# Performance work log

Measured on AMD Instinct MI355X. Metric: run time of the kernel, lower is better.

Reference implementation:

```python
import jax, jax.numpy as jnp
import numpy as np

BITS = 50

def _xor(a, b):
    # binary XOR on {0,1} floats: a + b - 2ab
    return a + b - 2.0 * a * b

def _maj(a, b, c):
    # majority (carry-out of a full adder) on {0,1} floats
    return a * b + a * c + b * c - 2.0 * a * b * c

def setup_inputs() -> dict:
    key = jax.random.key(0)
    kA, kB = jax.random.split(key)
    N = 1_000_000
    A = jax.random.randint(kA, (N, BITS), 0, 2).astype(jnp.float32)
    B = jax.random.randint(kB, (N, BITS), 0, 2).astype(jnp.float32)
    return {"A": A, "B": B}

def reference(A, B):
    """A - B via two's complement ripple-carry: A + NOT(B) + 1, LSB first.
    Returns (result [..., 50], borrow [..., 1])."""
    not_b = 1.0 - B                      # VecNOT
    # scan over the 50 bits (sequential carry dependency)
    a_bits = jnp.moveaxis(A, -1, 0)      # [50, N]
    b_bits = jnp.moveaxis(not_b, -1, 0)  # [50, N]
    c0 = jnp.ones(A.shape[:-1], dtype=A.dtype)  # initial carry = 1

    def step(c, ab):
        a, b = ab
        s = _xor(_xor(a, b), c)          # FullAdder sum
        c_next = _maj(a, b, c)           # FullAdder carry
        return c_next, s

    c_final, sums = jax.lax.scan(step, c0, (a_bits, b_bits))
    result = jnp.moveaxis(sums, 0, -1)   # [N, 50]
    borrow = (1.0 - c_final)[..., None]  # borrow_not(carry), [N, 1]
    return result, borrow
```

## Files before the change

### kernel.cpp

```cpp
#include <hip/hip_runtime.h>


constexpr int BITS = 50;
constexpr unsigned long long MASK50 = (1ULL << BITS) - 1ULL;

__device__ inline unsigned long long shfl64(unsigned long long v, int src) {
    int lo = __shfl((int)(unsigned)(v & 0xffffffffULL), src, 64);
    int hi = __shfl((int)(unsigned)(v >> 32), src, 64);
    return ((unsigned long long)(unsigned)hi << 32) | (unsigned long long)(unsigned)lo;
}

__global__ __launch_bounds__(256) void Subtractor50Bit_kernel(
    const float* __restrict__ A, const float* __restrict__ B,
    float* __restrict__ out, int N)
{
    const int lane = threadIdx.x & 63;
    const int wv   = threadIdx.x >> 6;
    const long long waveIdx = (long long)blockIdx.x * 4 + wv;
    const long long rowBase = waveIdx * 64;
    if (rowBase >= N) return;

    if (rowBase + 64 <= N) {
        const long long eBase = rowBase * BITS;
        const float* pa = A + eBase + lane;
        const float* pb = B + eBase + lane;

        float fa[BITS], fb[BITS];
        #pragma unroll
        for (int j = 0; j < BITS; ++j) fa[j] = pa[(long long)j * 64];
        #pragma unroll
        for (int j = 0; j < BITS; ++j) fb[j] = pb[(long long)j * 64];

        unsigned long long wa = 0, wb = 0;
        #pragma unroll
        for (int j = 0; j < BITS; ++j) {
            unsigned long long ma = __ballot(fa[j] != 0.0f);
            unsigned long long mb = __ballot(fb[j] != 0.0f);
            if (lane == j) { wa = ma; wb = mb; }
        }

        const int p0   = BITS * lane;
        const int idx0 = p0 >> 6;
        const int sh   = p0 & 63;
        unsigned long long a0 = shfl64(wa, idx0);
        unsigned long long a1 = shfl64(wa, idx0 + 1);
        unsigned long long b0 = shfl64(wb, idx0);
        unsigned long long b1 = shfl64(wb, idx0 + 1);

        unsigned long long av = a0 >> sh;
        unsigned long long bv = b0 >> sh;
        if (sh > 64 - BITS) {
            av |= a1 << (64 - sh);
            bv |= b1 << (64 - sh);
        }
        av &= MASK50;
        bv &= MASK50;

        unsigned long long diff = (av - bv) & MASK50;
        float borrow = (av < bv) ? 1.0f : 0.0f;

        #pragma unroll
        for (int j = 0; j < BITS; ++j) {
            int local = j * 64 + lane;
            int r     = local / BITS;
            int bit   = local - r * BITS;
            unsigned long long dr = shfl64(diff, r);
            out[eBase + local] = (float)((dr >> bit) & 1ULL);
        }
        out[(long long)N * BITS + rowBase + lane] = borrow;
    } else {
        long long r = rowBase + lane;
        if (r < N) {
            unsigned long long av = 0, bv = 0;
            for (int k = 0; k < BITS; ++k) {
                av |= (unsigned long long)(A[r * BITS + k] != 0.0f) << k;
                bv |= (unsigned long long)(B[r * BITS + k] != 0.0f) << k;
            }
            unsigned long long diff = (av - bv) & MASK50;
            for (int k = 0; k < BITS; ++k)
                out[r * BITS + k] = (float)((diff >> k) & 1ULL);
            out[(long long)N * BITS + r] = (av < bv) ? 1.0f : 0.0f;
        }
    }
}

extern "C" void kernel_launch(void* const* d_in, const int* in_sizes, int n_in,
                              void* d_out, int out_size, void* d_ws, size_t ws_size,
                              hipStream_t stream) {
    const float* A = (const float*)d_in[0];
    const float* B = (const float*)d_in[1];
    float* out = (float*)d_out;
    const int N = in_sizes[0] / BITS;

    const int waves  = (N + 63) / 64;
    const int blocks = (waves + 3) / 4;
    Subtractor50Bit_kernel<<<blocks, 256, 0, stream>>>(A, B, out, N);
}
```

Baseline: 447.6 us.

## Use persistent grid-stride waves with register prefetch of the next tile

Replaces the one-wave-per-64-row launch with a fixed grid of 1024 blocks whose waves loop over tiles. Each wave issues the loads for its next tile before doing the ballot, shuffle and store work on the current one, so memory latency overlaps with compute. The tail rows are handled by block 0. Holding two sets of 100 float registers may raise register pressure, and the launch_bounds hint of 2 may limit occupancy on this memory-bound kernel.

Measured after the change: 457.1 us. 1.02x slower.

```diff
diff --git a/kernel.cpp b/kernel.cpp
--- a/kernel.cpp
+++ b/kernel.cpp
@@ -3,6 +3,8 @@
 
 constexpr int BITS = 50;
 constexpr unsigned long long MASK50 = (1ULL << BITS) - 1ULL;
+constexpr int ROWS_PER_TILE = 64;
+constexpr int ELEMS_PER_TILE = ROWS_PER_TILE * BITS;
 
 __device__ inline unsigned long long shfl64(unsigned long long v, int src) {
     int lo = __shfl((int)(unsigned)(v & 0xffffffffULL), src, 64);
@@ -10,27 +12,47 @@
     return ((unsigned long long)(unsigned)hi << 32) | (unsigned long long)(unsigned)lo;
 }
 
-__global__ __launch_bounds__(256) void Subtractor50Bit_kernel(
+__global__ __launch_bounds__(256, 2) void Subtractor50Bit_kernel(
     const float* __restrict__ A, const float* __restrict__ B,
-    float* __restrict__ out, int N)
+    float* __restrict__ out, int N, int numTiles, int waveStride)
 {
     const int lane = threadIdx.x & 63;
-    const int wv   = threadIdx.x >> 6;
-    const long long waveIdx = (long long)blockIdx.x * 4 + wv;
-    const long long rowBase = waveIdx * 64;
-    if (rowBase >= N) return;
 
-    if (rowBase + 64 <= N) {
-        const long long eBase = rowBase * BITS;
-        const float* pa = A + eBase + lane;
-        const float* pb = B + eBase + lane;
+    if (blockIdx.x == 0 && threadIdx.x < 64) {
+        long long r = (long long)numTiles * ROWS_PER_TILE + lane;
+        if (r < N) {
+            unsigned long long av = 0, bv = 0;
+            for (int k = 0; k < BITS; ++k) {
+                av |= (unsigned long long)(A[r * BITS + k] != 0.0f) << k;
+                bv |= (unsigned long long)(B[r * BITS + k] != 0.0f) << k;
+            }
+            unsigned long long diff = (av - bv) & MASK50;
+            for (int k = 0; k < BITS; ++k)
+                out[r * BITS + k] = (float)((diff >> k) & 1ULL);
+            out[(long long)N * BITS + r] = (av < bv) ? 1.0f : 0.0f;
+        }
+    }
 
-        float fa[BITS], fb[BITS];
+    long long t = (long long)blockIdx.x * 4 + (threadIdx.x >> 6);
+    if (t >= numTiles) return;
+
+    const int p0   = BITS * lane;
+    const int idx0 = p0 >> 6;
+    const int sh   = p0 & 63;
+    const long long borrowBase = (long long)N * BITS;
+
+    float fa[BITS], fb[BITS];
+    {
+        const float* pa = A + t * ELEMS_PER_TILE + lane;
+        const float* pb = B + t * ELEMS_PER_TILE + lane;
         #pragma unroll
-        for (int j = 0; j < BITS; ++j) fa[j] = pa[(long long)j * 64];
-        #pragma unroll
-        for (int j = 0; j < BITS; ++j) fb[j] = pb[(long long)j * 64];
+        for (int j = 0; j < BITS; ++j) {
+            fa[j] = pa[j * 64];
+            fb[j] = pb[j * 64];
+        }
+    }
 
+    for (;;) {
         unsigned long long wa = 0, wb = 0;
         #pragma unroll
         for (int j = 0; j < BITS; ++j) {
@@ -39,9 +61,20 @@
             if (lane == j) { wa = ma; wb = mb; }
         }
 
-        const int p0   = BITS * lane;
-        const int idx0 = p0 >> 6;
-        const int sh   = p0 & 63;
+        const long long eBase = t * ELEMS_PER_TILE;
+        const long long nt    = t + waveStride;
+        const bool more       = nt < numTiles;
+
+        if (more) {
+            const float* pa = A + nt * ELEMS_PER_TILE + lane;
+            const float* pb = B + nt * ELEMS_PER_TILE + lane;
+            #pragma unroll
+            for (int j = 0; j < BITS; ++j) {
+                fa[j] = pa[j * 64];
+                fb[j] = pb[j * 64];
+            }
+        }
+
         unsigned long long a0 = shfl64(wa, idx0);
         unsigned long long a1 = shfl64(wa, idx0 + 1);
         unsigned long long b0 = shfl64(wb, idx0);
@@ -67,20 +100,10 @@
             unsigned long long dr = shfl64(diff, r);
             out[eBase + local] = (float)((dr >> bit) & 1ULL);
         }
-        out[(long long)N * BITS + rowBase + lane] = borrow;
-    } else {
-        long long r = rowBase + lane;
-        if (r < N) {
-            unsigned long long av = 0, bv = 0;
-            for (int k = 0; k < BITS; ++k) {
-                av |= (unsigned long long)(A[r * BITS + k] != 0.0f) << k;
-                bv |= (unsigned long long)(B[r * BITS + k] != 0.0f) << k;
-            }
-            unsigned long long diff = (av - bv) & MASK50;
-            for (int k = 0; k < BITS; ++k)
-                out[r * BITS + k] = (float)((diff >> k) & 1ULL);
-            out[(long long)N * BITS + r] = (av < bv) ? 1.0f : 0.0f;
-        }
+        out[borrowBase + t * ROWS_PER_TILE + lane] = borrow;
+
+        if (!more) break;
+        t = nt;
     }
 }
 
@@ -92,7 +115,8 @@
     float* out = (float*)d_out;
     const int N = in_sizes[0] / BITS;
 
-    const int waves  = (N + 63) / 64;
-    const int blocks = (waves + 3) / 4;
-    Subtractor50Bit_kernel<<<blocks, 256, 0, stream>>>(A, B, out, N);
+    const int numTiles   = N / ROWS_PER_TILE;
+    const int blocks     = 1024;
+    const int waveStride = blocks * 4;
+    Subtractor50Bit_kernel<<<blocks, 256, 0, stream>>>(A, B, out, N, numTiles, waveStride);
 }
```
